# Optimization experiments

Hardware: AMD Instinct MI355X
Metric: run time of the kernel (lower is better)

The kernel has to match this reference:

```python
import jax, jax.numpy as jnp
import numpy as np


def _layer_norm(x, w, b, eps=1e-5):
    mu = jnp.mean(x, axis=-1, keepdims=True)
    xc = x - mu
    var = jnp.mean(xc * xc, axis=-1, keepdims=True)
    return xc * jax.lax.rsqrt(var + eps) * w + b


def setup_inputs() -> dict:
    key = jax.random.key(0)
    ks = jax.random.split(key, 6)
    S, B, H = 2048, 2, 1024
    NH, NKV, HD = 16, 4, 64
    E, K, F = 8, 2, 4096
    w = lambda k, shape: 0.02 * jax.random.normal(k, shape, dtype=jnp.float32)
    return {
        "hidden_states": jax.random.normal(ks[0], (S, B, H), dtype=jnp.float32),
        "ln1_weight": jnp.ones((H,), jnp.float32),
        "ln1_bias": jnp.zeros((H,), jnp.float32),
        "ln2_weight": jnp.ones((H,), jnp.float32),
        "ln2_bias": jnp.zeros((H,), jnp.float32),
        "qkv_weight": w(ks[1], (H, (NH + 2 * NKV) * HD)),
        "proj_weight": w(ks[2], (H, H)),
        "router_weight": w(ks[3], (H, E)),
        "moe_w1": w(ks[4], (E, H, F)),
        "moe_w2": w(ks[5], (E, F, H)),
        "num_heads": NH,
        "num_kv_heads": NKV,
        "top_k": K,
    }


def reference(hidden_states, ln1_weight, ln1_bias, ln2_weight, ln2_bias,
              qkv_weight, proj_weight, router_weight, moe_w1, moe_w2,
              num_heads, num_kv_heads, top_k):
    S, B, H = hidden_states.shape
    HD = H // num_heads
    scale = 1.0 / (HD ** 0.5)

    # --- LN1 -> QKV projection (GQA split) ---
    ln1 = _layer_norm(hidden_states, ln1_weight, ln1_bias)
    qkv = ln1 @ qkv_weight                               # [S,B,(NH+2NKV)*HD]
    q_end = num_heads * HD
    k_end = q_end + num_kv_heads * HD
    q = qkv[..., :q_end].reshape(S, B, num_heads, HD)
    k = qkv[..., q_end:k_end].reshape(S, B, num_kv_heads, HD)
    v = qkv[..., k_end:].reshape(S, B, num_kv_heads, HD)
    rep = num_heads // num_kv_heads                      # repeat_interleave on head dim
    k = jnp.repeat(k, rep, axis=2)
    v = jnp.repeat(v, rep, axis=2)

    # --- causal SDPA, layout [B,NH,S,HD] ---
    q_bf = q.transpose(1, 2, 0, 3)
    k_bf = k.transpose(1, 2, 0, 3)
    v_bf = v.transpose(1, 2, 0, 3)
    scores = jnp.einsum('bhqd,bhkd->bhqk', q_bf, k_bf) * scale
    causal = jnp.tril(jnp.ones((S, S), dtype=bool))
    scores = jnp.where(causal, scores, jnp.finfo(scores.dtype).min)
    p = jax.nn.softmax(scores, axis=-1)
    attn = jnp.einsum('bhqk,bhkd->bhqd', p, v_bf)
    attn_out = attn.transpose(2, 0, 1, 3).reshape(S, B, H)  # back to [S,B,H]

    # --- output projection + residual ---
    h_attn = hidden_states + attn_out @ proj_weight

    # --- LN2 -> router top-k -> expert FFN -> weighted combine ---
    ln2 = _layer_norm(h_attn, ln2_weight, ln2_bias)
    T = S * B
    x = ln2.reshape(T, H)
    logits = x @ router_weight                           # [T,E]
    probs = jax.nn.softmax(logits, axis=-1)
    top_p, top_i = jax.lax.top_k(probs, top_k)           # [T,K]

    def expert_fn(_, w):
        w1, w2 = w
        return None, jax.nn.gelu(x @ w1, approximate=False) @ w2  # [T,H]

    _, outs = jax.lax.scan(expert_fn, None, (moe_w1, moe_w2))     # [E,T,H]
    gathered = outs[top_i, jnp.arange(T)[:, None], :]             # [T,K,H]
    moe_out = jnp.sum(gathered * top_p[..., None].astype(outs.dtype), axis=1)

    return h_attn + moe_out.reshape(S, B, H)
```

## Files before the change

kernel.cpp:

```cpp
#include <hip/hip_runtime.h>
#include <hip/hip_bf16.h>

constexpr int TT   = 4096;
constexpr int HH   = 1024;
constexpr int QKVN = 1536;
constexpr int FF   = 4096;

using f16x8  = __attribute__((ext_vector_type(8))) _Float16;
using f16x4  = __attribute__((ext_vector_type(4))) _Float16;
using bf16x8 = __attribute__((ext_vector_type(8))) short;
using s16x4  = __attribute__((ext_vector_type(4))) short;
using f32x4  = __attribute__((ext_vector_type(4))) float;

static __device__ __forceinline__ f32x4 mfma16(f16x8 a, f16x8 b, f32x4 c) {
  return __builtin_amdgcn_mfma_f32_16x16x32_f16(a, b, c, 0, 0, 0);
}
static __device__ __forceinline__ f32x4 mfmabf(bf16x8 a, bf16x8 b, f32x4 c) {
  return __builtin_amdgcn_mfma_f32_16x16x32_bf16(a, b, c, 0, 0, 0);
}
static __device__ __forceinline__ short f2bf(float f) {
  union { float f; unsigned u; } v; v.f = f;
  unsigned r = v.u + 0x7fffu + ((v.u >> 16) & 1u);
  return (short)(r >> 16);
}
static __device__ __forceinline__ void split16(float f, _Float16 &h, _Float16 &l) {
  _Float16 hh = (_Float16)f; h = hh; l = (_Float16)(f - (float)hh);
}
static __device__ __forceinline__ float fast_gelu(float x) {
  float u = 0.7978845608f * (x + 0.044715f * x * x * x);
  float a = __expf(-2.0f * fabsf(u));
  float t = (1.0f - a) * __builtin_amdgcn_rcpf(1.0f + a);
  t = copysignf(t, u);
  return 0.5f * x * (1.0f + t);
}
static __device__ __forceinline__ void gload16(const void* g, void* l) {
  __builtin_amdgcn_global_load_lds((__attribute__((address_space(1))) void*)(g),
                                   (__attribute__((address_space(3))) void*)(l), 16, 0, 0);
}

__global__ void zero_cnt(int* cnt) { if (threadIdx.x < 8) cnt[threadIdx.x] = 0; }

__global__ __launch_bounds__(256) void wconv_split(const float* __restrict__ W,
    _Float16* __restrict__ oh, _Float16* __restrict__ ol, int K, int N)
{
  __shared__ float ts[64][68];
  int n0 = blockIdx.x * 64, k0 = blockIdx.y * 64, t = threadIdx.x;
  #pragma unroll
  for (int it = 0; it < 4; it++) {
    int el = it * 1024 + t * 4; int r = el >> 6, c = el & 63;
    float4 v = *(const float4*)&W[(size_t)(k0 + r) * N + n0 + c];
    *(float4*)&ts[r][c] = v;
  }
  __syncthreads();
  #pragma unroll
  for (int it = 0; it < 4; it++) {
    int el = it * 1024 + t * 4; int nr = el >> 6, kc = el & 63;
    f16x4 hv, lv;
    #pragma unroll
    for (int q = 0; q < 4; q++) { _Float16 hh, ll; split16(ts[kc + q][nr], hh, ll); hv[q] = hh; lv[q] = ll; }
    size_t o = (size_t)(n0 + nr) * K + k0 + kc;
    *(f16x4*)&oh[o] = hv; *(f16x4*)&ol[o] = lv;
  }
}

__global__ __launch_bounds__(256) void wconv_bf(const float* __restrict__ W,
    short* __restrict__ o, int K, int N)
{
  __shared__ float ts[64][68];
  const float* Wz = W + (size_t)blockIdx.z * K * N;
  short* oz = o + (size_t)blockIdx.z * K * N;
  int n0 = blockIdx.x * 64, k0 = blockIdx.y * 64, t = threadIdx.x;
  #pragma unroll
  for (int it = 0; it < 4; it++) {
    int el = it * 1024 + t * 4; int r = el >> 6, c = el & 63;
    float4 v = *(const float4*)&Wz[(size_t)(k0 + r) * N + n0 + c];
    *(float4*)&ts[r][c] = v;
  }
  __syncthreads();
  #pragma unroll
  for (int it = 0; it < 4; it++) {
    int el = it * 1024 + t * 4; int nr = el >> 6, kc = el & 63;
    s16x4 bv;
    #pragma unroll
    for (int q = 0; q < 4; q++) bv[q] = f2bf(ts[kc + q][nr]);
    *(s16x4*)&oz[(size_t)(n0 + nr) * K + k0 + kc] = bv;
  }
}

__global__ __launch_bounds__(256) void vtrans(const float* __restrict__ qkv,
    _Float16* __restrict__ vh, _Float16* __restrict__ vl)
{
  __shared__ float ts[64][68];
  int bkv = blockIdx.x, b = bkv >> 2, kvh = bkv & 3;
  int s0 = blockIdx.y * 64, t = threadIdx.x;
  #pragma unroll
  for (int it = 0; it < 4; it++) {
    int el = it * 1024 + t * 4; int r = el >> 6, c = el & 63;
    float4 v = *(const float4*)&qkv[(size_t)((s0 + r) * 2 + b) * QKVN + 1280 + kvh * 64 + c];
    *(float4*)&ts[r][c] = v;
  }
  __syncthreads();
  #pragma unroll
  for (int it = 0; it < 4; it++) {
    int el = it * 1024 + t * 4; int d = el >> 6, sc = el & 63;
    f16x4 hv, lv;
    #pragma unroll
    for (int q = 0; q < 4; q++) { _Float16 hh, ll; split16(ts[sc + q][d], hh, ll); hv[q] = hh; lv[q] = ll; }
    size_t o = ((size_t)bkv * 64 + d) * 2048 + s0 + sc;
    *(f16x4*)&vh[o] = hv; *(f16x4*)&vl[o] = lv;
  }
}

template<int MODE>
__global__ __launch_bounds__(256) void ln_split(const float* __restrict__ in,
    const float* __restrict__ wt, const float* __restrict__ bs,
    _Float16* __restrict__ oh, _Float16* __restrict__ ol,
    float* __restrict__ xo, short* __restrict__ xbo)
{
  int row = blockIdx.x, tid = threadIdx.x;
  const float4* ip = (const float4*)(in + (size_t)row * HH);
  float4 v = ip[tid];
  float s = v.x + v.y + v.z + v.w;
  #pragma unroll
  for (int m = 1; m < 64; m <<= 1) s += __shfl_xor(s, m, 64);
  __shared__ float red1[4], red2[4];
  int wid = tid >> 6;
  if ((tid & 63) == 0) red1[wid] = s;
  __syncthreads();
  float mu = (red1[0] + red1[1] + red1[2] + red1[3]) * (1.0f / HH);
  float4 c; c.x = v.x - mu; c.y = v.y - mu; c.z = v.z - mu; c.w = v.w - mu;
  float s2 = c.x*c.x + c.y*c.y + c.z*c.z + c.w*c.w;
  #pragma unroll
  for (int m = 1; m < 64; m <<= 1) s2 += __shfl_xor(s2, m, 64);
  if ((tid & 63) == 0) red2[wid] = s2;
  __syncthreads();
  float ve = (red2[0] + red2[1] + red2[2] + red2[3]) * (1.0f / HH) + 1e-5f;
  float rs = rsqrtf(ve);
  rs = rs * (1.5f - 0.5f * ve * rs * rs);
  float4 wv = ((const float4*)wt)[tid], bv = ((const float4*)bs)[tid];
  float o4[4];
  o4[0] = c.x * rs * wv.x + bv.x; o4[1] = c.y * rs * wv.y + bv.y;
  o4[2] = c.z * rs * wv.z + bv.z; o4[3] = c.w * rs * wv.w + bv.w;
  size_t base = (size_t)row * HH + tid * 4;
  if (MODE == 0) {
    f16x4 hv, lv;
    #pragma unroll
    for (int q = 0; q < 4; q++) { _Float16 hh, ll; split16(o4[q], hh, ll); hv[q] = hh; lv[q] = ll; }
    *(f16x4*)&oh[base] = hv; *(f16x4*)&ol[base] = lv;
  } else {
    float4 ov; ov.x = o4[0]; ov.y = o4[1]; ov.z = o4[2]; ov.w = o4[3];
    *(float4*)&xo[base] = ov;
    s16x4 bvv;
    #pragma unroll
    for (int q = 0; q < 4; q++) bvv[q] = f2bf(o4[q]);
    *(s16x4*)&xbo[base] = bvv;
  }
}

template<int EPI>
__global__ __launch_bounds__(256) void gemm_split2(
    const _Float16* __restrict__ Agh, const _Float16* __restrict__ Agl,
    const _Float16* __restrict__ Bgh, const _Float16* __restrict__ Bgl,
    int K, float* __restrict__ C, int ldc, const float* __restrict__ resid,
    _Float16* __restrict__ kh, _Float16* __restrict__ kl)
{
  __shared__ _Float16 AhS[4096], AlS[4096], BhS[4096], BlS[4096];
  const int tid = threadIdx.x, lane = tid & 63, w = tid >> 6;
  const int wr = w >> 1, wc = w & 1;
  const int m0 = blockIdx.y * 128, n0 = blockIdx.x * 128;
  f32x4 acc[4][4] = {};
  const _Float16 *pah[2], *pal[2], *pbh[2], *pbl[2];
  int ldsb[2];
  #pragma unroll
  for (int i = 0; i < 2; i++) {
    int E = i * 2048 + w * 512 + lane * 8;
    int r = E >> 5, cc = E & 31;
    int cs = cc ^ ((r & 3) << 3);
    pah[i] = Agh + (size_t)(m0 + r) * K + cs;
    pal[i] = Agl + (size_t)(m0 + r) * K + cs;
    pbh[i] = Bgh + (size_t)(n0 + r) * K + cs;
    pbl[i] = Bgl + (size_t)(n0 + r) * K + cs;
    ldsb[i] = i * 2048 + w * 512;
  }
  const int rr = lane & 15, ko = (lane >> 4) * 8;
  const int xo = (rr & 3) << 3;
  for (int k0 = 0; k0 < K; k0 += 32) {
    __syncthreads();
    #pragma unroll
    for (int i = 0; i < 2; i++) {
      gload16(pah[i] + k0, &AhS[ldsb[i]]);
      gload16(pal[i] + k0, &AlS[ldsb[i]]);
      gload16(pbh[i] + k0, &BhS[ldsb[i]]);
      gload16(pbl[i] + k0, &BlS[ldsb[i]]);
    }
    __syncthreads();
    f16x8 fah[4], fal[4], fbh[4], fbl[4];
    #pragma unroll
    for (int m = 0; m < 4; m++) {
      int ro = (wr * 64 + m * 16 + rr) * 32 + (ko ^ xo);
      fah[m] = *(const f16x8*)&AhS[ro];
      fal[m] = *(const f16x8*)&AlS[ro];
    }
    #pragma unroll
    for (int n = 0; n < 4; n++) {
      int ro = (wc * 64 + n * 16 + rr) * 32 + (ko ^ xo);
      fbh[n] = *(const f16x8*)&BhS[ro];
      fbl[n] = *(const f16x8*)&BlS[ro];
    }
    #pragma unroll
    for (int m = 0; m < 4; m++)
      #pragma unroll
      for (int n = 0; n < 4; n++) {
        acc[m][n] = mfma16(fah[m], fbh[n], acc[m][n]);
        acc[m][n] = mfma16(fah[m], fbl[n], acc[m][n]);
        acc[m][n] = mfma16(fal[m], fbh[n], acc[m][n]);
      }
  }
  int r0 = m0 + wr * 64 + (lane >> 4) * 4;
  int c0 = n0 + wc * 64 + (lane & 15);
  #pragma unroll
  for (int m = 0; m < 4; m++)
    #pragma unroll
    for (int n = 0; n < 4; n++)
      #pragma unroll
      for (int j = 0; j < 4; j++) {
        int tr = r0 + m * 16 + j, tc = c0 + n * 16;
        size_t idx = (size_t)tr * ldc + tc;
        float v = acc[m][n][j];
        if (EPI == 1) v += resid[idx];
        C[idx] = v;
        if (EPI == 0 && tc >= 1024 && tc < 1280) {
          int s = tr >> 1, bb = tr & 1;
          int kvh = (tc - 1024) >> 6, d = (tc - 1024) & 63;
          _Float16 hh, ll; split16(v, hh, ll);
          size_t kidx = ((size_t)(bb * 4 + kvh) * 2048 + s) * 64 + d;
          kh[kidx] = hh; kl[kidx] = ll;
        }
      }
}

__global__ __launch_bounds__(256) void attn2(const float* __restrict__ qkv,
    const _Float16* __restrict__ khg, const _Float16* __restrict__ klg,
    const _Float16* __restrict__ vhg, const _Float16* __restrict__ vlg,
    _Float16* __restrict__ aoh, _Float16* __restrict__ aol)
{
  __shared__ _Float16 KhS[4096], KlS[4096], VhS[4096], VlS[4096];
  __shared__ _Float16 Ph[64][72], Pl[64][72];
  int bh = blockIdx.x;
  int qt = gridDim.y - 1 - blockIdx.y;
  int h = bh >> 1, b = bh & 1, kvh = h >> 2, bkv = b * 4 + kvh;
  int q0 = qt * 64;
  int tid = threadIdx.x, lane = tid & 63, w = tid >> 6;
  int rr = lane & 15, ko = (lane >> 4) * 8;
  const int xo8 = (rr & 7) << 3;
  int qrow = q0 + w * 16 + rr;
  const float* qp = qkv + (size_t)(qrow * 2 + b) * QKVN + h * 64;
  f16x8 qh[2], ql[2];
  #pragma unroll
  for (int kk = 0; kk < 2; kk++) {
    const float4* p = (const float4*)(qp + kk * 32 + ko);
    float4 v0 = p[0], v1 = p[1];
    float tq[8] = {v0.x, v0.y, v0.z, v0.w, v1.x, v1.y, v1.z, v1.w};
    f16x8 hv, lv;
    #pragma unroll
    for (int q = 0; q < 8; q++) { _Float16 hh, ll; split16(tq[q], hh, ll); hv[q] = hh; lv[q] = ll; }
    qh[kk] = hv; ql[kk] = lv;
  }
  const _Float16 *pk[2][2], *pv[2][2];
  int ldsb[2];
  #pragma unroll
  for (int i = 0; i < 2; i++) {
    int E = i * 2048 + w * 512 + lane * 8;
    int r = E >> 6, cc = E & 63;
    int cs = cc ^ ((r & 7) << 3);
    pk[i][0] = khg + ((size_t)bkv * 2048 + r) * 64 + cs;
    pk[i][1] = klg + ((size_t)bkv * 2048 + r) * 64 + cs;
    pv[i][0] = vhg + ((size_t)bkv * 64 + r) * 2048 + cs;
    pv[i][1] = vlg + ((size_t)bkv * 64 + r) * 2048 + cs;
    ldsb[i] = i * 2048 + w * 512;
  }
  f32x4 o[4] = {};
  float mo[4] = {-1e30f, -1e30f, -1e30f, -1e30f};
  float lo[4] = {0.f, 0.f, 0.f, 0.f};
  for (int ks = 0; ks <= q0; ks += 64) {
    __syncthreads();
    #pragma unroll
    for (int i = 0; i < 2; i++) {
      gload16(pk[i][0] + (size_t)ks * 64, &KhS[ldsb[i]]);
      gload16(pk[i][1] + (size_t)ks * 64, &KlS[ldsb[i]]);
      gload16(pv[i][0] + ks, &VhS[ldsb[i]]);
      gload16(pv[i][1] + ks, &VlS[ldsb[i]]);
    }
    __syncthreads();
    f32x4 s[4] = {};
    __builtin_amdgcn_s_setprio(1);
    #pragma unroll
    for (int n = 0; n < 4; n++)
      #pragma unroll
      for (int kk = 0; kk < 2; kk++) {
        int ro = (n * 16 + rr) * 64 + ((kk * 32 + ko) ^ xo8);
        f16x8 kbh = *(const f16x8*)&KhS[ro];
        f16x8 kbl = *(const f16x8*)&KlS[ro];
        s[n] = mfma16(qh[kk], kbh, s[n]);
        s[n] = mfma16(qh[kk], kbl, s[n]);
        s[n] = mfma16(ql[kk], kbh, s[n]);
      }
    __builtin_amdgcn_s_setprio(0);
    bool diag = (ks == q0);
    int myrow = q0 + w * 16 + (lane >> 4) * 4;
    #pragma unroll
    for (int n = 0; n < 4; n++)
      #pragma unroll
      for (int j = 0; j < 4; j++) {
        float v = s[n][j] * 0.125f;
        if (diag && (ks + n * 16 + rr) > (myrow + j)) v = -1e30f;
        s[n][j] = v;
      }
    float mt[4];
    #pragma unroll
    for (int j = 0; j < 4; j++) mt[j] = fmaxf(fmaxf(s[0][j], s[1][j]), fmaxf(s[2][j], s[3][j]));
    #pragma unroll
    for (int msk = 1; msk < 16; msk <<= 1)
      #pragma unroll
      for (int j = 0; j < 4; j++) mt[j] = fmaxf(mt[j], __shfl_xor(mt[j], msk, 64));
    float pvv[4][4], rsum[4];
    #pragma unroll
    for (int j = 0; j < 4; j++) {
      float mn = fmaxf(mo[j], mt[j]);
      float al = expf(mo[j] - mn);
      mo[j] = mn;
      rsum[j] = 0.f;
      #pragma unroll
      for (int n = 0; n < 4; n++) { float pp = expf(s[n][j] - mn); pvv[n][j] = pp; rsum[j] += pp; }
      lo[j] *= al;
      #pragma unroll
      for (int n = 0; n < 4; n++) o[n][j] *= al;
    }
    #pragma unroll
    for (int msk = 1; msk < 16; msk <<= 1)
      #pragma unroll
      for (int j = 0; j < 4; j++) rsum[j] += __shfl_xor(rsum[j], msk, 64);
    #pragma unroll
    for (int j = 0; j < 4; j++) lo[j] += rsum[j];
    int prow = w * 16 + (lane >> 4) * 4;
    #pragma unroll
    for (int n = 0; n < 4; n++)
      #pragma unroll
      for (int j = 0; j < 4; j++) {
        _Float16 hh, ll; split16(pvv[n][j], hh, ll);
        Ph[prow + j][n * 16 + rr] = hh;
        Pl[prow + j][n * 16 + rr] = ll;
      }
    __builtin_amdgcn_s_setprio(1);
    #pragma unroll
    for (int kk = 0; kk < 2; kk++) {
      f16x8 pah = *(const f16x8*)&Ph[w * 16 + rr][kk * 32 + ko];
      f16x8 pal = *(const f16x8*)&Pl[w * 16 + rr][kk * 32 + ko];
      #pragma unroll
      for (int dn = 0; dn < 4; dn++) {
        int ro = (dn * 16 + rr) * 64 + ((kk * 32 + ko) ^ xo8);
        f16x8 vbh = *(const f16x8*)&VhS[ro];
        f16x8 vbl = *(const f16x8*)&VlS[ro];
        o[dn] = mfma16(pah, vbh, o[dn]);
        o[dn] = mfma16(pah, vbl, o[dn]);
        o[dn] = mfma16(pal, vbh, o[dn]);
      }
    }
    __builtin_amdgcn_s_setprio(0);
  }
  float inv[4];
  #pragma unroll
  for (int j = 0; j < 4; j++) inv[j] = 1.0f / lo[j];
  int orow = q0 + w * 16 + (lane >> 4) * 4;
  int ocol = h * 64 + rr;
  #pragma unroll
  for (int dn = 0; dn < 4; dn++)
    #pragma unroll
    for (int j = 0; j < 4; j++) {
      float v = o[dn][j] * inv[j];
      _Float16 hh, ll; split16(v, hh, ll);
      size_t idx = (size_t)((orow + j) * 2 + b) * HH + ocol + dn * 16;
      aoh[idx] = hh; aol[idx] = ll;
    }
}

__global__ __launch_bounds__(256) void router_kernel(const float* __restrict__ x,
    const float* __restrict__ rw, int* __restrict__ list, float* __restrict__ listp,
    int* __restrict__ cnt)
{
  __shared__ float rws[HH * 8];
  int tid = threadIdx.x;
  for (int i = tid; i < HH * 8; i += 256) rws[i] = rw[i];
  __syncthreads();
  int t = blockIdx.x * 4 + (tid >> 6);
  int lane = tid & 63;
  const float* xp = x + (size_t)t * HH;
  float acc[8] = {};
  for (int i = lane; i < HH; i += 64) {
    float xv = xp[i];
    #pragma unroll
    for (int e = 0; e < 8; e++) acc[e] += xv * rws[i * 8 + e];
  }
  #pragma unroll
  for (int e = 0; e < 8; e++)
    #pragma unroll
    for (int m = 1; m < 64; m <<= 1) acc[e] += __shfl_xor(acc[e], m, 64);
  if (lane == 0) {
    float mx = acc[0];
    #pragma unroll
    for (int e = 1; e < 8; e++) mx = fmaxf(mx, acc[e]);
    float p[8], sum = 0.f;
    #pragma unroll
    for (int e = 0; e < 8; e++) { p[e] = expf(acc[e] - mx); sum += p[e]; }
    float inv = 1.0f / sum;
    int i1 = 0; float v1 = acc[0];
    #pragma unroll
    for (int e = 1; e < 8; e++) if (acc[e] > v1) { v1 = acc[e]; i1 = e; }
    int i2 = -1; float v2 = -3.4e38f;
    #pragma unroll
    for (int e = 0; e < 8; e++) if (e != i1 && acc[e] > v2) { v2 = acc[e]; i2 = e; }
    int pos1 = atomicAdd(&cnt[i1], 1);
    list[i1 * TT + pos1] = t; listp[i1 * TT + pos1] = p[i1] * inv;
    int pos2 = atomicAdd(&cnt[i2], 1);
    list[i2 * TT + pos2] = t; listp[i2 * TT + pos2] = p[i2] * inv;
  }
}

__global__ __launch_bounds__(256) void moe1_full(const short* __restrict__ xbf,
    const short* __restrict__ w1T, const int* __restrict__ list,
    const int* __restrict__ cnt, short* __restrict__ hidden)
{
  int id = blockIdx.x;
  int e = id & 7;
  int inner = id >> 3;
  int mx = inner & 31, nx = inner >> 5;
  int ce = cnt[e];
  int m0 = mx * 128;
  if (m0 >= ce) return;
  int n0 = nx * 128;
  int off = 0;
  #pragma unroll
  for (int i = 0; i < 8; i++) if (i < e) off += cnt[i];
  __shared__ short AS[8192], BS[8192];
  const int tid = threadIdx.x, lane = tid & 63, w = tid >> 6;
  const int wr = w >> 1, wc = w & 1;
  f32x4 acc[4][4] = {};
  const short *pa[4], *pb[4];
  int ldsb[4];
  #pragma unroll
  for (int i = 0; i < 4; i++) {
    int E = i * 2048 + w * 512 + lane * 8;
    int r = E >> 6, c = E & 63;
    int cs = c ^ ((r & 7) << 3);
    int apos = m0 + r; if (apos > ce - 1) apos = ce - 1;
    int tok = list[e * TT + apos];
    pa[i] = xbf + (size_t)tok * HH + cs;
    pb[i] = w1T + ((size_t)e * FF + n0 + r) * HH + cs;
    ldsb[i] = E;
  }
  const int rr = lane & 15, ko = (lane >> 4) * 8;
  const int xo = (rr & 7) << 3;
  for (int k0 = 0; k0 < HH; k0 += 64) {
    __syncthreads();
    #pragma unroll
    for (int i = 0; i < 4; i++) {
      gload16(pa[i] + k0, &AS[ldsb[i]]);
      gload16(pb[i] + k0, &BS[ldsb[i]]);
    }
    __syncthreads();
    #pragma unroll
    for (int kk = 0; kk < 2; kk++) {
      bf16x8 fa[4], fb[4];
      #pragma unroll
      for (int m = 0; m < 4; m++) fa[m] = *(const bf16x8*)&AS[(wr * 64 + m * 16 + rr) * 64 + ((kk * 32 + ko) ^ xo)];
      #pragma unroll
      for (int n = 0; n < 4; n++) fb[n] = *(const bf16x8*)&BS[(wc * 64 + n * 16 + rr) * 64 + ((kk * 32 + ko) ^ xo)];
      #pragma unroll
      for (int m = 0; m < 4; m++)
        #pragma unroll
        for (int n = 0; n < 4; n++) acc[m][n] = mfmabf(fa[m], fb[n], acc[m][n]);
    }
  }
  int p0 = m0 + wr * 64 + (lane >> 4) * 4;
  int c0 = n0 + wc * 64 + (lane & 15);
  #pragma unroll
  for (int m = 0; m < 4; m++)
    #pragma unroll
    for (int n = 0; n < 4; n++)
      #pragma unroll
      for (int j = 0; j < 4; j++) {
        int pos = p0 + m * 16 + j;
        if (pos < ce) {
          float v = fast_gelu(acc[m][n][j]);
          hidden[(size_t)(off + pos) * FF + c0 + n * 16] = f2bf(v);
        }
      }
}

__global__ __launch_bounds__(256) void moe2_full(const short* __restrict__ hidden,
    const short* __restrict__ w2T, const int* __restrict__ list,
    const float* __restrict__ listp, const int* __restrict__ cnt,
    float* __restrict__ outp)
{
  int id = blockIdx.x;
  int e = id & 7;
  int inner = id >> 3;
  int mx = inner & 31, nx = inner >> 5;
  int ce = cnt[e];
  int m0 = mx * 128;
  if (m0 >= ce) return;
  int n0 = nx * 128;
  int off = 0;
  #pragma unroll
  for (int i = 0; i < 8; i++) if (i < e) off += cnt[i];
  __shared__ short AS[2][8192], BS[2][8192];
  const int tid = threadIdx.x, lane = tid & 63, w = tid >> 6;
  const int wr = w >> 1, wc = w & 1;
  f32x4 acc[4][4] = {};
  const short *pa[4], *pb[4];
  int ldsb[4];
  #pragma unroll
  for (int i = 0; i < 4; i++) {
    int E = i * 2048 + w * 512 + lane * 8;
    int r = E >> 6, c = E & 63;
    int cs = c ^ ((r & 7) << 3);
    int apos = m0 + r; if (apos > ce - 1) apos = ce - 1;
    pa[i] = hidden + ((size_t)off + apos) * FF + cs;
    pb[i] = w2T + ((size_t)e * HH + n0 + r) * FF + cs;
    ldsb[i] = E;
  }
  const int rr = lane & 15, ko = (lane >> 4) * 8;
  const int xo = (rr & 7) << 3;
  #pragma unroll
  for (int i = 0; i < 4; i++) {
    gload16(pa[i], &AS[0][ldsb[i]]);
    gload16(pb[i], &BS[0][ldsb[i]]);
  }
  __syncthreads();
  int cb = 0;
  for (int k0 = 0; k0 < FF; k0 += 64) {
    int nk = k0 + 64;
    if (nk < FF) {
      #pragma unroll
      for (int i = 0; i < 4; i++) {
        gload16(pa[i] + nk, &AS[cb ^ 1][ldsb[i]]);
        gload16(pb[i] + nk, &BS[cb ^ 1][ldsb[i]]);
      }
    }
    __builtin_amdgcn_s_setprio(1);
    #pragma unroll
    for (int kk = 0; kk < 2; kk++) {
      bf16x8 fa[4], fb[4];
      #pragma unroll
      for (int m = 0; m < 4; m++) fa[m] = *(const bf16x8*)&AS[cb][(wr * 64 + m * 16 + rr) * 64 + ((kk * 32 + ko) ^ xo)];
      #pragma unroll
      for (int n = 0; n < 4; n++) fb[n] = *(const bf16x8*)&BS[cb][(wc * 64 + n * 16 + rr) * 64 + ((kk * 32 + ko) ^ xo)];
      #pragma unroll
      for (int m = 0; m < 4; m++)
        #pragma unroll
        for (int n = 0; n < 4; n++) acc[m][n] = mfmabf(fa[m], fb[n], acc[m][n]);
    }
    __builtin_amdgcn_s_setprio(0);
    __syncthreads();
    cb ^= 1;
  }
  int p0 = m0 + wr * 64 + (lane >> 4) * 4;
  int c0 = n0 + wc * 64 + (lane & 15);
  #pragma unroll
  for (int m = 0; m < 4; m++)
    #pragma unroll
    for (int j = 0; j < 4; j++) {
      int pos = p0 + m * 16 + j;
      if (pos < ce) {
        int tk = list[e * TT + pos];
        float pw = listp[e * TT + pos];
        #pragma unroll
        for (int n = 0; n < 4; n++)
          atomicAdd(&outp[(size_t)tk * HH + c0 + n * 16], pw * acc[m][n][j]);
      }
    }
}

__global__ __launch_bounds__(256) void moe_gemm1(const float* __restrict__ x,
    const float* __restrict__ w1, const int* __restrict__ list,
    const int* __restrict__ cnt, short* __restrict__ hidden, int e)
{
  int ce = cnt[e];
  int m0 = blockIdx.y * 128;
  if (m0 >= ce) return;
  int n0 = blockIdx.x * 128;
  __shared__ short As[128][40], Bs[128][40];
  int tid = threadIdx.x, lane = tid & 63, w = tid >> 6, wr = w >> 1, wc = w & 1;
  f32x4 acc[4][4] = {};
  int arow = tid >> 1, akh = (tid & 1) * 16;
  int apos = m0 + arow;
  int tok = list[(size_t)e * TT + (apos < ce ? apos : 0)];
  const float* ap = x + (size_t)tok * HH + akh;
  int bn = tid & 127, bkh = (tid >> 7) * 16;
  const float* bp = w1 + (size_t)e * HH * FF + (size_t)bkh * FF + n0 + bn;
  for (int k0 = 0; k0 < HH; k0 += 32) {
    __syncthreads();
    {
      const float4* p = (const float4*)(ap + k0);
      bf16x8 s0, s1;
      #pragma unroll
      for (int q = 0; q < 2; q++) { float4 v = p[q]; s0[q*4] = f2bf(v.x); s0[q*4+1] = f2bf(v.y); s0[q*4+2] = f2bf(v.z); s0[q*4+3] = f2bf(v.w); }
      #pragma unroll
      for (int q = 0; q < 2; q++) { float4 v = p[q+2]; s1[q*4] = f2bf(v.x); s1[q*4+1] = f2bf(v.y); s1[q*4+2] = f2bf(v.z); s1[q*4+3] = f2bf(v.w); }
      *(bf16x8*)&As[arow][akh] = s0; *(bf16x8*)&As[arow][akh+8] = s1;
    }
    {
      const float* p = bp + (size_t)k0 * FF;
      bf16x8 s0, s1;
      #pragma unroll
      for (int q = 0; q < 8; q++) s0[q] = f2bf(p[(size_t)q * FF]);
      #pragma unroll
      for (int q = 0; q < 8; q++) s1[q] = f2bf(p[(size_t)(q+8) * FF]);
      *(bf16x8*)&Bs[bn][bkh] = s0; *(bf16x8*)&Bs[bn][bkh+8] = s1;
    }
    __syncthreads();
    int rr = lane & 15, ko = (lane >> 4) * 8;
    bf16x8 fa[4], fb[4];
    #pragma unroll
    for (int m = 0; m < 4; m++) fa[m] = *(bf16x8*)&As[wr*64 + m*16 + rr][ko];
    #pragma unroll
    for (int n = 0; n < 4; n++) fb[n] = *(bf16x8*)&Bs[wc*64 + n*16 + rr][ko];
    #pragma unroll
    for (int m = 0; m < 4; m++)
      #pragma unroll
      for (int n = 0; n < 4; n++) acc[m][n] = mfmabf(fa[m], fb[n], acc[m][n]);
  }
  int p0 = m0 + wr*64 + (lane >> 4) * 4;
  int c0 = n0 + wc*64 + (lane & 15);
  #pragma unroll
  for (int m = 0; m < 4; m++)
    #pragma unroll
    for (int n = 0; n < 4; n++)
      #pragma unroll
      for (int j = 0; j < 4; j++) {
        int pos = p0 + m*16 + j;
        if (pos < ce) {
          float v = acc[m][n][j];
          v = 0.5f * v * (1.0f + erff(v * 0.70710678f));
          hidden[(size_t)pos * FF + c0 + n*16] = f2bf(v);
        }
      }
}

__global__ __launch_bounds__(256) void moe_gemm2(const short* __restrict__ hidden,
    const float* __restrict__ w2, const int* __restrict__ list,
    const float* __restrict__ listp, const int* __restrict__ cnt,
    float* __restrict__ outp, int e)
{
  int ce = cnt[e];
  int m0 = blockIdx.y * 128;
  if (m0 >= ce) return;
  int n0 = blockIdx.x * 128;
  __shared__ short As[128][40], Bs[128][40];
  int tid = threadIdx.x, lane = tid & 63, w = tid >> 6, wr = w >> 1, wc = w & 1;
  f32x4 acc[4][4] = {};
  int arow = tid >> 1, akh = (tid & 1) * 16;
  int apos = m0 + arow;
  const short* ap = hidden + (size_t)(apos < ce ? apos : 0) * FF + akh;
  int bn = tid & 127, bkh = (tid >> 7) * 16;
  const float* bp = w2 + (size_t)e * FF * HH + (size_t)bkh * HH + n0 + bn;
  for (int k0 = 0; k0 < FF; k0 += 32) {
    __syncthreads();
    {
      const int4* p = (const int4*)(ap + k0);
      int4 a0 = p[0], a1 = p[1];
      *(int4*)&As[arow][akh]   = a0;
      *(int4*)&As[arow][akh+8] = a1;
    }
    {
      const float* p = bp + (size_t)k0 * HH;
      bf16x8 s0, s1;
      #pragma unroll
      for (int q = 0; q < 8; q++) s0[q] = f2bf(p[(size_t)q * HH]);
      #pragma unroll
      for (int q = 0; q < 8; q++) s1[q] = f2bf(p[(size_t)(q+8) * HH]);
      *(bf16x8*)&Bs[bn][bkh] = s0; *(bf16x8*)&Bs[bn][bkh+8] = s1;
    }
    __syncthreads();
    int rr = lane & 15, ko = (lane >> 4) * 8;
    bf16x8 fa[4], fb[4];
    #pragma unroll
    for (int m = 0; m < 4; m++) fa[m] = *(bf16x8*)&As[wr*64 + m*16 + rr][ko];
    #pragma unroll
    for (int n = 0; n < 4; n++) fb[n] = *(bf16x8*)&Bs[wc*64 + n*16 + rr][ko];
    #pragma unroll
    for (int m = 0; m < 4; m++)
      #pragma unroll
      for (int n = 0; n < 4; n++) acc[m][n] = mfmabf(fa[m], fb[n], acc[m][n]);
  }
  int p0 = m0 + wr*64 + (lane >> 4) * 4;
  int c0 = n0 + wc*64 + (lane & 15);
  #pragma unroll
  for (int m = 0; m < 4; m++)
    #pragma unroll
    for (int j = 0; j < 4; j++) {
      int pos = p0 + m*16 + j;
      if (pos < ce) {
        int tk = list[(size_t)e * TT + pos];
        float pw = listp[(size_t)e * TT + pos];
        #pragma unroll
        for (int n = 0; n < 4; n++)
          atomicAdd(&outp[(size_t)tk * HH + c0 + n*16], pw * acc[m][n][j]);
      }
    }
}

extern "C" void kernel_launch(void* const* d_in, const int* in_sizes, int n_in,
                              void* d_out, int out_size, void* d_ws, size_t ws_size,
                              hipStream_t stream)
{
  const float* hs      = (const float*)d_in[0];
  const float* ln1w    = (const float*)d_in[1];
  const float* ln1b    = (const float*)d_in[2];
  const float* ln2w    = (const float*)d_in[3];
  const float* ln2b    = (const float*)d_in[4];
  const float* qkvw    = (const float*)d_in[5];
  const float* projw   = (const float*)d_in[6];
  const float* routerw = (const float*)d_in[7];
  const float* w1      = (const float*)d_in[8];
  const float* w2      = (const float*)d_in[9];
  float* out = (float*)d_out;

  const size_t MB = 1024 * 1024;
  char* wsb = (char*)d_ws;
  bool full = ws_size >= 153 * MB;

  float*    qkvbuf = (float*)wsb;
  _Float16* khb    = (_Float16*)(wsb + 24 * MB);
  _Float16* klb    = (_Float16*)(wsb + 26 * MB);
  _Float16* vhb    = (_Float16*)(wsb + 28 * MB);
  _Float16* vlb    = (_Float16*)(wsb + 30 * MB);
  short*    hidden = (short*)wsb;
  size_t r2 = full ? 64 * MB : 32 * MB;
  _Float16* ln1h = (_Float16*)(wsb + r2);
  _Float16* ln1l = (_Float16*)(wsb + r2 + 8 * MB);
  _Float16* aohb = ln1h;
  _Float16* aolb = ln1l;
  float*    xbuf = (float*)(wsb + r2);
  short*    xbf  = (short*)(wsb + r2 + 16 * MB);
  size_t r3 = full ? 88 * MB : 56 * MB;
  _Float16* qkvwTh  = (_Float16*)(wsb + r3);
  _Float16* qkvwTl  = (_Float16*)(wsb + r3 + 3 * MB);
  _Float16* projwTh = (_Float16*)(wsb + r3 + 6 * MB);
  _Float16* projwTl = (_Float16*)(wsb + r3 + 8 * MB);
  short*    w1T     = (short*)(wsb + r3);
  short*    w2T     = (short*)(wsb + r3);
  size_t r4 = full ? 152 * MB : 66 * MB;
  int*   list  = (int*)(wsb + r4);
  float* listp = (float*)(wsb + r4 + 128 * 1024);
  int*   cnt   = (int*)(wsb + r4 + 256 * 1024);

  zero_cnt<<<1, 64, 0, stream>>>(cnt);
  wconv_split<<<dim3(QKVN / 64, HH / 64), 256, 0, stream>>>(qkvw, qkvwTh, qkvwTl, HH, QKVN);
  wconv_split<<<dim3(HH / 64, HH / 64), 256, 0, stream>>>(projw, projwTh, projwTl, HH, HH);
  ln_split<0><<<TT, 256, 0, stream>>>(hs, ln1w, ln1b, ln1h, ln1l, nullptr, nullptr);
  gemm_split2<0><<<dim3(QKVN / 128, TT / 128), 256, 0, stream>>>(
      ln1h, ln1l, qkvwTh, qkvwTl, HH, qkvbuf, QKVN, nullptr, khb, klb);
  vtrans<<<dim3(8, 32), 256, 0, stream>>>(qkvbuf, vhb, vlb);
  attn2<<<dim3(32, 32), 256, 0, stream>>>(qkvbuf, khb, klb, vhb, vlb, aohb, aolb);
  gemm_split2<1><<<dim3(HH / 128, TT / 128), 256, 0, stream>>>(
      aohb, aolb, projwTh, projwTl, HH, out, HH, hs, nullptr, nullptr);
  ln_split<1><<<TT, 256, 0, stream>>>(out, ln2w, ln2b, nullptr, nullptr, xbuf, xbf);
  router_kernel<<<TT / 4, 256, 0, stream>>>(xbuf, routerw, list, listp, cnt);
  if (full) {
    wconv_bf<<<dim3(FF / 64, HH / 64, 8), 256, 0, stream>>>(w1, w1T, HH, FF);
    moe1_full<<<8 * 32 * 32, 256, 0, stream>>>(xbf, w1T, list, cnt, hidden);
    wconv_bf<<<dim3(HH / 64, FF / 64, 8), 256, 0, stream>>>(w2, w2T, FF, HH);
    moe2_full<<<8 * 32 * 8, 256, 0, stream>>>(hidden, w2T, list, listp, cnt, out);
  } else {
    for (int e = 0; e < 8; e++) {
      moe_gemm1<<<dim3(FF / 128, TT / 128), 256, 0, stream>>>(xbuf, w1, list, cnt, hidden, e);
      moe_gemm2<<<dim3(HH / 128, TT / 128), 256, 0, stream>>>(hidden, w2, list, listp, cnt, out, e);
    }
  }
}
```

Before: 690.7 us.

## Enlarge MoE expert GEMM tiles to 256x256 with 512 threads and split-K

```diff
diff --git a/kernel.cpp b/kernel.cpp
--- a/kernel.cpp
+++ b/kernel.cpp
@@ -426,65 +426,84 @@
   }
 }
 
-__global__ __launch_bounds__(256) void moe1_full(const short* __restrict__ xbf,
+
+__global__ __launch_bounds__(512, 2) void moe1_g2(const short* __restrict__ xbf,
     const short* __restrict__ w1T, const int* __restrict__ list,
     const int* __restrict__ cnt, short* __restrict__ hidden)
 {
+  __shared__ short LDS[2][16384];
   int id = blockIdx.x;
   int e = id & 7;
   int inner = id >> 3;
-  int mx = inner & 31, nx = inner >> 5;
+  int mx = inner & 15, nx = inner >> 4;
   int ce = cnt[e];
-  int m0 = mx * 128;
+  int m0 = mx * 256;
   if (m0 >= ce) return;
-  int n0 = nx * 128;
+  int n0 = nx * 256;
   int off = 0;
   #pragma unroll
   for (int i = 0; i < 8; i++) if (i < e) off += cnt[i];
-  __shared__ short AS[8192], BS[8192];
   const int tid = threadIdx.x, lane = tid & 63, w = tid >> 6;
-  const int wr = w >> 1, wc = w & 1;
-  f32x4 acc[4][4] = {};
-  const short *pa[4], *pb[4];
-  int ldsb[4];
-  #pragma unroll
-  for (int i = 0; i < 4; i++) {
-    int E = i * 2048 + w * 512 + lane * 8;
-    int r = E >> 6, c = E & 63;
-    int cs = c ^ ((r & 7) << 3);
-    int apos = m0 + r; if (apos > ce - 1) apos = ce - 1;
-    int tok = list[e * TT + apos];
-    pa[i] = xbf + (size_t)tok * HH + cs;
-    pb[i] = w1T + ((size_t)e * FF + n0 + r) * HH + cs;
-    ldsb[i] = E;
-  }
-  const int rr = lane & 15, ko = (lane >> 4) * 8;
-  const int xo = (rr & 7) << 3;
-  for (int k0 = 0; k0 < HH; k0 += 64) {
-    __syncthreads();
-    #pragma unroll
-    for (int i = 0; i < 4; i++) {
-      gload16(pa[i] + k0, &AS[ldsb[i]]);
-      gload16(pb[i] + k0, &BS[ldsb[i]]);
-    }
-    __syncthreads();
-    #pragma unroll
-    for (int kk = 0; kk < 2; kk++) {
-      bf16x8 fa[4], fb[4];
-      #pragma unroll
-      for (int m = 0; m < 4; m++) fa[m] = *(const bf16x8*)&AS[(wr * 64 + m * 16 + rr) * 64 + ((kk * 32 + ko) ^ xo)];
-      #pragma unroll
-      for (int n = 0; n < 4; n++) fb[n] = *(const bf16x8*)&BS[(wc * 64 + n * 16 + rr) * 64 + ((kk * 32 + ko) ^ xo)];
-      #pragma unroll
-      for (int m = 0; m < 4; m++)
-        #pragma unroll
-        for (int n = 0; n < 4; n++) acc[m][n] = mfmabf(fa[m], fb[n], acc[m][n]);
-    }
-  }
-  int p0 = m0 + wr * 64 + (lane >> 4) * 4;
+  const int wr = w >> 2, wc = w & 3;
+  f32x4 acc[8][4] = {};
+  const short *pa[2], *pb[2];
+  int lof[4];
+  {
+    int rowr = tid >> 2;
+    int colr = (tid & 3) * 8;
+    #pragma unroll
+    for (int i = 0; i < 2; i++) {
+      int row = i * 128 + rowr;
+      int cs = colr ^ ((row & 3) << 3);
+      int apos = m0 + row; if (apos > ce - 1) apos = ce - 1;
+      int tok = list[e * TT + apos];
+      pa[i] = xbf + (size_t)tok * HH + cs;
+      pb[i] = w1T + ((size_t)e * FF + n0 + row) * HH + cs;
+      lof[i] = i * 4096 + tid * 8;
+      lof[2 + i] = 8192 + i * 4096 + tid * 8;
+    }
+  }
+  const int rr = lane & 15, koX = ((lane >> 4) * 8) ^ ((rr & 3) << 3);
+  const int T = HH / 32;
+  #pragma unroll
+  for (int i = 0; i < 2; i++) {
+    gload16(pa[i], &LDS[0][lof[i]]);
+    gload16(pb[i], &LDS[0][lof[2 + i]]);
+  }
+  int cb = 0;
+  for (int t = 0; t < T; t++) {
+    if (t + 1 < T) {
+      int k0 = (t + 1) * 32;
+      #pragma unroll
+      for (int i = 0; i < 2; i++) {
+        gload16(pa[i] + k0, &LDS[cb ^ 1][lof[i]]);
+        gload16(pb[i] + k0, &LDS[cb ^ 1][lof[2 + i]]);
+      }
+      asm volatile("s_waitcnt vmcnt(4)" ::: "memory");
+    } else {
+      asm volatile("s_waitcnt vmcnt(0)" ::: "memory");
+    }
+    __builtin_amdgcn_s_barrier();
+    __builtin_amdgcn_sched_barrier(0);
+    const short* As = &LDS[cb][0];
+    bf16x8 fa[8], fb[4];
+    #pragma unroll
+    for (int m = 0; m < 8; m++) fa[m] = *(const bf16x8*)&As[(wr * 128 + m * 16 + rr) * 32 + koX];
+    #pragma unroll
+    for (int n = 0; n < 4; n++) fb[n] = *(const bf16x8*)&As[8192 + (wc * 64 + n * 16 + rr) * 32 + koX];
+    #pragma unroll
+    for (int m = 0; m < 8; m++)
+      #pragma unroll
+      for (int n = 0; n < 4; n++) acc[m][n] = mfmabf(fa[m], fb[n], acc[m][n]);
+    asm volatile("s_waitcnt lgkmcnt(0)" ::: "memory");
+    __builtin_amdgcn_s_barrier();
+    __builtin_amdgcn_sched_barrier(0);
+    cb ^= 1;
+  }
+  int p0 = m0 + wr * 128 + (lane >> 4) * 4;
   int c0 = n0 + wc * 64 + (lane & 15);
   #pragma unroll
-  for (int m = 0; m < 4; m++)
+  for (int m = 0; m < 8; m++)
     #pragma unroll
     for (int n = 0; n < 4; n++)
       #pragma unroll
@@ -497,77 +516,84 @@
       }
 }
 
-__global__ __launch_bounds__(256) void moe2_full(const short* __restrict__ hidden,
+__global__ __launch_bounds__(512, 2) void moe2_g2(const short* __restrict__ hidden,
     const short* __restrict__ w2T, const int* __restrict__ list,
     const float* __restrict__ listp, const int* __restrict__ cnt,
     float* __restrict__ outp)
 {
+  __shared__ short LDS[2][16384];
   int id = blockIdx.x;
   int e = id & 7;
-  int inner = id >> 3;
-  int mx = inner & 31, nx = inner >> 5;
+  int r0_ = id >> 3;
+  int mx = r0_ & 15, nx = (r0_ >> 4) & 3, ksp = r0_ >> 6;
   int ce = cnt[e];
-  int m0 = mx * 128;
+  int m0 = mx * 256;
   if (m0 >= ce) return;
-  int n0 = nx * 128;
+  int n0 = nx * 256;
+  int kbase = ksp * (FF / 2);
   int off = 0;
   #pragma unroll
   for (int i = 0; i < 8; i++) if (i < e) off += cnt[i];
-  __shared__ short AS[2][8192], BS[2][8192];
   const int tid = threadIdx.x, lane = tid & 63, w = tid >> 6;
-  const int wr = w >> 1, wc = w & 1;
-  f32x4 acc[4][4] = {};
-  const short *pa[4], *pb[4];
-  int ldsb[4];
-  #pragma unroll
-  for (int i = 0; i < 4; i++) {
-    int E = i * 2048 + w * 512 + lane * 8;
-    int r = E >> 6, c = E & 63;
-    int cs = c ^ ((r & 7) << 3);
-    int apos = m0 + r; if (apos > ce - 1) apos = ce - 1;
-    pa[i] = hidden + ((size_t)off + apos) * FF + cs;
-    pb[i] = w2T + ((size_t)e * HH + n0 + r) * FF + cs;
-    ldsb[i] = E;
-  }
-  const int rr = lane & 15, ko = (lane >> 4) * 8;
-  const int xo = (rr & 7) << 3;
-  #pragma unroll
-  for (int i = 0; i < 4; i++) {
-    gload16(pa[i], &AS[0][ldsb[i]]);
-    gload16(pb[i], &BS[0][ldsb[i]]);
-  }
-  __syncthreads();
+  const int wr = w >> 2, wc = w & 3;
+  f32x4 acc[8][4] = {};
+  const short *pa[2], *pb[2];
+  int lof[4];
+  {
+    int rowr = tid >> 2;
+    int colr = (tid & 3) * 8;
+    #pragma unroll
+    for (int i = 0; i < 2; i++) {
+      int row = i * 128 + rowr;
+      int cs = colr ^ ((row & 3) << 3);
+      int apos = m0 + row; if (apos > ce - 1) apos = ce - 1;
+      pa[i] = hidden + ((size_t)off + apos) * FF + kbase + cs;
+      pb[i] = w2T + ((size_t)e * HH + n0 + row) * FF + kbase + cs;
+      lof[i] = i * 4096 + tid * 8;
+      lof[2 + i] = 8192 + i * 4096 + tid * 8;
+    }
+  }
+  const int rr = lane & 15, koX = ((lane >> 4) * 8) ^ ((rr & 3) << 3);
+  const int T = (FF / 2) / 32;
+  #pragma unroll
+  for (int i = 0; i < 2; i++) {
+    gload16(pa[i], &LDS[0][lof[i]]);
+    gload16(pb[i], &LDS[0][lof[2 + i]]);
+  }
   int cb = 0;
-  for (int k0 = 0; k0 < FF; k0 += 64) {
-    int nk = k0 + 64;
-    if (nk < FF) {
-      #pragma unroll
-      for (int i = 0; i < 4; i++) {
-        gload16(pa[i] + nk, &AS[cb ^ 1][ldsb[i]]);
-        gload16(pb[i] + nk, &BS[cb ^ 1][ldsb[i]]);
-      }
-    }
-    __builtin_amdgcn_s_setprio(1);
-    #pragma unroll
-    for (int kk = 0; kk < 2; kk++) {
-      bf16x8 fa[4], fb[4];
-      #pragma unroll
-      for (int m = 0; m < 4; m++) fa[m] = *(const bf16x8*)&AS[cb][(wr * 64 + m * 16 + rr) * 64 + ((kk * 32 + ko) ^ xo)];
-      #pragma unroll
-      for (int n = 0; n < 4; n++) fb[n] = *(const bf16x8*)&BS[cb][(wc * 64 + n * 16 + rr) * 64 + ((kk * 32 + ko) ^ xo)];
-      #pragma unroll
-      for (int m = 0; m < 4; m++)
-        #pragma unroll
-        for (int n = 0; n < 4; n++) acc[m][n] = mfmabf(fa[m], fb[n], acc[m][n]);
-    }
-    __builtin_amdgcn_s_setprio(0);
-    __syncthreads();
+  for (int t = 0; t < T; t++) {
+    if (t + 1 < T) {
+      int k0 = (t + 1) * 32;
+      #pragma unroll
+      for (int i = 0; i < 2; i++) {
+        gload16(pa[i] + k0, &LDS[cb ^ 1][lof[i]]);
+        gload16(pb[i] + k0, &LDS[cb ^ 1][lof[2 + i]]);
+      }
+      asm volatile("s_waitcnt vmcnt(4)" ::: "memory");
+    } else {
+      asm volatile("s_waitcnt vmcnt(0)" ::: "memory");
+    }
+    __builtin_amdgcn_s_barrier();
+    __builtin_amdgcn_sched_barrier(0);
+    const short* As = &LDS[cb][0];
+    bf16x8 fa[8], fb[4];
+    #pragma unroll
+    for (int m = 0; m < 8; m++) fa[m] = *(const bf16x8*)&As[(wr * 128 + m * 16 + rr) * 32 + koX];
+    #pragma unroll
+    for (int n = 0; n < 4; n++) fb[n] = *(const bf16x8*)&As[8192 + (wc * 64 + n * 16 + rr) * 32 + koX];
+    #pragma unroll
+    for (int m = 0; m < 8; m++)
+      #pragma unroll
+      for (int n = 0; n < 4; n++) acc[m][n] = mfmabf(fa[m], fb[n], acc[m][n]);
+    asm volatile("s_waitcnt lgkmcnt(0)" ::: "memory");
+    __builtin_amdgcn_s_barrier();
+    __builtin_amdgcn_sched_barrier(0);
     cb ^= 1;
   }
-  int p0 = m0 + wr * 64 + (lane >> 4) * 4;
+  int p0 = m0 + wr * 128 + (lane >> 4) * 4;
   int c0 = n0 + wc * 64 + (lane & 15);
   #pragma unroll
-  for (int m = 0; m < 4; m++)
+  for (int m = 0; m < 8; m++)
     #pragma unroll
     for (int j = 0; j < 4; j++) {
       int pos = p0 + m * 16 + j;
@@ -769,9 +795,9 @@
   router_kernel<<<TT / 4, 256, 0, stream>>>(xbuf, routerw, list, listp, cnt);
   if (full) {
     wconv_bf<<<dim3(FF / 64, HH / 64, 8), 256, 0, stream>>>(w1, w1T, HH, FF);
-    moe1_full<<<8 * 32 * 32, 256, 0, stream>>>(xbf, w1T, list, cnt, hidden);
+    moe1_g2<<<8 * 16 * 16, 512, 0, stream>>>(xbf, w1T, list, cnt, hidden);
     wconv_bf<<<dim3(HH / 64, FF / 64, 8), 256, 0, stream>>>(w2, w2T, FF, HH);
-    moe2_full<<<8 * 32 * 8, 256, 0, stream>>>(hidden, w2T, list, listp, cnt, out);
+    moe2_g2<<<8 * 16 * 4 * 2, 512, 0, stream>>>(hidden, w2T, list, listp, cnt, out);
   } else {
     for (int e = 0; e < 8; e++) {
       moe_gemm1<<<dim3(FF / 128, TT / 128), 256, 0, stream>>>(xbuf, w1, list, cnt, hidden, e);
```

After: 735.5 us. +6.5%, slower.

## Double-buffer MoE GEMMs with BK=32 tiles, split-K expert down-projection, new LDS swizzle

Applied to the files above, without the earlier changes.

```diff
diff --git a/kernel.cpp b/kernel.cpp
--- a/kernel.cpp
+++ b/kernel.cpp
@@ -175,7 +175,7 @@
   for (int i = 0; i < 2; i++) {
     int E = i * 2048 + w * 512 + lane * 8;
     int r = E >> 5, cc = E & 31;
-    int cs = cc ^ ((r & 3) << 3);
+    int cs = cc ^ (((r >> 2) & 3) << 3);
     pah[i] = Agh + (size_t)(m0 + r) * K + cs;
     pal[i] = Agl + (size_t)(m0 + r) * K + cs;
     pbh[i] = Bgh + (size_t)(n0 + r) * K + cs;
@@ -183,7 +183,7 @@
     ldsb[i] = i * 2048 + w * 512;
   }
   const int rr = lane & 15, ko = (lane >> 4) * 8;
-  const int xo = (rr & 3) << 3;
+  const int xo = ((rr >> 2) & 3) << 3;
   for (int k0 = 0; k0 < K; k0 += 32) {
     __syncthreads();
     #pragma unroll
@@ -426,10 +426,12 @@
   }
 }
 
-__global__ __launch_bounds__(256) void moe1_full(const short* __restrict__ xbf,
+
+__global__ __launch_bounds__(256) void moe1_p2(const short* __restrict__ xbf,
     const short* __restrict__ w1T, const int* __restrict__ list,
     const int* __restrict__ cnt, short* __restrict__ hidden)
 {
+  __shared__ short A2[2][4096], B2[2][4096];
   int id = blockIdx.x;
   int e = id & 7;
   int inner = id >> 3;
@@ -441,45 +443,60 @@
   int off = 0;
   #pragma unroll
   for (int i = 0; i < 8; i++) if (i < e) off += cnt[i];
-  __shared__ short AS[8192], BS[8192];
   const int tid = threadIdx.x, lane = tid & 63, w = tid >> 6;
   const int wr = w >> 1, wc = w & 1;
   f32x4 acc[4][4] = {};
-  const short *pa[4], *pb[4];
-  int ldsb[4];
-  #pragma unroll
-  for (int i = 0; i < 4; i++) {
+  const short *pa[2], *pb[2];
+  int lof[2];
+  #pragma unroll
+  for (int i = 0; i < 2; i++) {
     int E = i * 2048 + w * 512 + lane * 8;
-    int r = E >> 6, c = E & 63;
-    int cs = c ^ ((r & 7) << 3);
+    int r = E >> 5, c = E & 31;
+    int cs = c ^ (((r >> 2) & 3) << 3);
     int apos = m0 + r; if (apos > ce - 1) apos = ce - 1;
     int tok = list[e * TT + apos];
     pa[i] = xbf + (size_t)tok * HH + cs;
     pb[i] = w1T + ((size_t)e * FF + n0 + r) * HH + cs;
-    ldsb[i] = E;
+    lof[i] = E;
   }
   const int rr = lane & 15, ko = (lane >> 4) * 8;
-  const int xo = (rr & 7) << 3;
-  for (int k0 = 0; k0 < HH; k0 += 64) {
-    __syncthreads();
-    #pragma unroll
-    for (int i = 0; i < 4; i++) {
-      gload16(pa[i] + k0, &AS[ldsb[i]]);
-      gload16(pb[i] + k0, &BS[ldsb[i]]);
-    }
-    __syncthreads();
-    #pragma unroll
-    for (int kk = 0; kk < 2; kk++) {
-      bf16x8 fa[4], fb[4];
-      #pragma unroll
-      for (int m = 0; m < 4; m++) fa[m] = *(const bf16x8*)&AS[(wr * 64 + m * 16 + rr) * 64 + ((kk * 32 + ko) ^ xo)];
-      #pragma unroll
-      for (int n = 0; n < 4; n++) fb[n] = *(const bf16x8*)&BS[(wc * 64 + n * 16 + rr) * 64 + ((kk * 32 + ko) ^ xo)];
-      #pragma unroll
-      for (int m = 0; m < 4; m++)
-        #pragma unroll
-        for (int n = 0; n < 4; n++) acc[m][n] = mfmabf(fa[m], fb[n], acc[m][n]);
-    }
+  const int koX = ko ^ (((rr >> 2) & 3) << 3);
+  const int T = HH / 32;
+  #pragma unroll
+  for (int i = 0; i < 2; i++) {
+    gload16(pa[i], &A2[0][lof[i]]);
+    gload16(pb[i], &B2[0][lof[i]]);
+  }
+  int cb = 0;
+  for (int t = 0; t < T; t++) {
+    if (t + 1 < T) {
+      int k0 = (t + 1) * 32;
+      #pragma unroll
+      for (int i = 0; i < 2; i++) {
+        gload16(pa[i] + k0, &A2[cb ^ 1][lof[i]]);
+        gload16(pb[i] + k0, &B2[cb ^ 1][lof[i]]);
+      }
+      asm volatile("s_waitcnt vmcnt(4)" ::: "memory");
+    } else {
+      asm volatile("s_waitcnt vmcnt(0)" ::: "memory");
+    }
+    __builtin_amdgcn_s_barrier();
+    __builtin_amdgcn_sched_barrier(0);
+    bf16x8 fa[4], fb[4];
+    #pragma unroll
+    for (int m = 0; m < 4; m++) fa[m] = *(const bf16x8*)&A2[cb][(wr * 64 + m * 16 + rr) * 32 + koX];
+    #pragma unroll
+    for (int n = 0; n < 4; n++) fb[n] = *(const bf16x8*)&B2[cb][(wc * 64 + n * 16 + rr) * 32 + koX];
+    __builtin_amdgcn_s_setprio(1);
+    #pragma unroll
+    for (int m = 0; m < 4; m++)
+      #pragma unroll
+      for (int n = 0; n < 4; n++) acc[m][n] = mfmabf(fa[m], fb[n], acc[m][n]);
+    __builtin_amdgcn_s_setprio(0);
+    asm volatile("s_waitcnt lgkmcnt(0)" ::: "memory");
+    __builtin_amdgcn_s_barrier();
+    __builtin_amdgcn_sched_barrier(0);
+    cb ^= 1;
   }
   int p0 = m0 + wr * 64 + (lane >> 4) * 4;
   int c0 = n0 + wc * 64 + (lane & 15);
@@ -497,71 +514,76 @@
       }
 }
 
-__global__ __launch_bounds__(256) void moe2_full(const short* __restrict__ hidden,
+__global__ __launch_bounds__(256) void moe2_p2(const short* __restrict__ hidden,
     const short* __restrict__ w2T, const int* __restrict__ list,
     const float* __restrict__ listp, const int* __restrict__ cnt,
     float* __restrict__ outp)
 {
+  __shared__ short A2[2][4096], B2[2][4096];
   int id = blockIdx.x;
   int e = id & 7;
-  int inner = id >> 3;
-  int mx = inner & 31, nx = inner >> 5;
+  int r_ = id >> 3;
+  int mx = r_ & 31, nx = (r_ >> 5) & 7, ksp = r_ >> 8;
   int ce = cnt[e];
   int m0 = mx * 128;
   if (m0 >= ce) return;
   int n0 = nx * 128;
+  int kbase = ksp * (FF / 2);
   int off = 0;
   #pragma unroll
   for (int i = 0; i < 8; i++) if (i < e) off += cnt[i];
-  __shared__ short AS[2][8192], BS[2][8192];
   const int tid = threadIdx.x, lane = tid & 63, w = tid >> 6;
   const int wr = w >> 1, wc = w & 1;
   f32x4 acc[4][4] = {};
-  const short *pa[4], *pb[4];
-  int ldsb[4];
-  #pragma unroll
-  for (int i = 0; i < 4; i++) {
+  const short *pa[2], *pb[2];
+  int lof[2];
+  #pragma unroll
+  for (int i = 0; i < 2; i++) {
     int E = i * 2048 + w * 512 + lane * 8;
-    int r = E >> 6, c = E & 63;
-    int cs = c ^ ((r & 7) << 3);
+    int r = E >> 5, c = E & 31;
+    int cs = c ^ (((r >> 2) & 3) << 3);
     int apos = m0 + r; if (apos > ce - 1) apos = ce - 1;
-    pa[i] = hidden + ((size_t)off + apos) * FF + cs;
-    pb[i] = w2T + ((size_t)e * HH + n0 + r) * FF + cs;
-    ldsb[i] = E;
+    pa[i] = hidden + ((size_t)off + apos) * FF + kbase + cs;
+    pb[i] = w2T + ((size_t)e * HH + n0 + r) * FF + kbase + cs;
+    lof[i] = E;
   }
   const int rr = lane & 15, ko = (lane >> 4) * 8;
-  const int xo = (rr & 7) << 3;
-  #pragma unroll
-  for (int i = 0; i < 4; i++) {
-    gload16(pa[i], &AS[0][ldsb[i]]);
-    gload16(pb[i], &BS[0][ldsb[i]]);
-  }
-  __syncthreads();
+  const int koX = ko ^ (((rr >> 2) & 3) << 3);
+  const int T = (FF / 2) / 32;
+  #pragma unroll
+  for (int i = 0; i < 2; i++) {
+    gload16(pa[i], &A2[0][lof[i]]);
+    gload16(pb[i], &B2[0][lof[i]]);
+  }
   int cb = 0;
-  for (int k0 = 0; k0 < FF; k0 += 64) {
-    int nk = k0 + 64;
-    if (nk < FF) {
-      #pragma unroll
-      for (int i = 0; i < 4; i++) {
-        gload16(pa[i] + nk, &AS[cb ^ 1][ldsb[i]]);
-        gload16(pb[i] + nk, &BS[cb ^ 1][ldsb[i]]);
-      }
-    }
+  for (int t = 0; t < T; t++) {
+    if (t + 1 < T) {
+      int k0 = (t + 1) * 32;
+      #pragma unroll
+      for (int i = 0; i < 2; i++) {
+        gload16(pa[i] + k0, &A2[cb ^ 1][lof[i]]);
+        gload16(pb[i] + k0, &B2[cb ^ 1][lof[i]]);
+      }
+      asm volatile("s_waitcnt vmcnt(4)" ::: "memory");
+    } else {
+      asm volatile("s_waitcnt vmcnt(0)" ::: "memory");
+    }
+    __builtin_amdgcn_s_barrier();
+    __builtin_amdgcn_sched_barrier(0);
+    bf16x8 fa[4], fb[4];
+    #pragma unroll
+    for (int m = 0; m < 4; m++) fa[m] = *(const bf16x8*)&A2[cb][(wr * 64 + m * 16 + rr) * 32 + koX];
+    #pragma unroll
+    for (int n = 0; n < 4; n++) fb[n] = *(const bf16x8*)&B2[cb][(wc * 64 + n * 16 + rr) * 32 + koX];
     __builtin_amdgcn_s_setprio(1);
     #pragma unroll
-    for (int kk = 0; kk < 2; kk++) {
-      bf16x8 fa[4], fb[4];
-      #pragma unroll
-      for (int m = 0; m < 4; m++) fa[m] = *(const bf16x8*)&AS[cb][(wr * 64 + m * 16 + rr) * 64 + ((kk * 32 + ko) ^ xo)];
-      #pragma unroll
-      for (int n = 0; n < 4; n++) fb[n] = *(const bf16x8*)&BS[cb][(wc * 64 + n * 16 + rr) * 64 + ((kk * 32 + ko) ^ xo)];
-      #pragma unroll
-      for (int m = 0; m < 4; m++)
-        #pragma unroll
-        for (int n = 0; n < 4; n++) acc[m][n] = mfmabf(fa[m], fb[n], acc[m][n]);
-    }
+    for (int m = 0; m < 4; m++)
+      #pragma unroll
+      for (int n = 0; n < 4; n++) acc[m][n] = mfmabf(fa[m], fb[n], acc[m][n]);
     __builtin_amdgcn_s_setprio(0);
-    __syncthreads();
+    asm volatile("s_waitcnt lgkmcnt(0)" ::: "memory");
+    __builtin_amdgcn_s_barrier();
+    __builtin_amdgcn_sched_barrier(0);
     cb ^= 1;
   }
   int p0 = m0 + wr * 64 + (lane >> 4) * 4;
@@ -769,9 +791,9 @@
   router_kernel<<<TT / 4, 256, 0, stream>>>(xbuf, routerw, list, listp, cnt);
   if (full) {
     wconv_bf<<<dim3(FF / 64, HH / 64, 8), 256, 0, stream>>>(w1, w1T, HH, FF);
-    moe1_full<<<8 * 32 * 32, 256, 0, stream>>>(xbf, w1T, list, cnt, hidden);
+    moe1_p2<<<8 * 32 * 32, 256, 0, stream>>>(xbf, w1T, list, cnt, hidden);
     wconv_bf<<<dim3(HH / 64, FF / 64, 8), 256, 0, stream>>>(w2, w2T, FF, HH);
-    moe2_full<<<8 * 32 * 8, 256, 0, stream>>>(hidden, w2T, list, listp, cnt, out);
+    moe2_p2<<<8 * 32 * 8 * 2, 256, 0, stream>>>(hidden, w2T, list, listp, cnt, out);
   } else {
     for (int e = 0; e < 8; e++) {
       moe_gemm1<<<dim3(FF / 128, TT / 128), 256, 0, stream>>>(xbuf, w1, list, cnt, hidden, e);
```

New measurement: 666.7 us. 1.04x faster.
